# Kernel tuning notes

Hardware: AMD Instinct MI355X
Metric: run time of the kernel (lower is better)

The kernel has to match this reference:

```python
import jax, jax.numpy as jnp
from jax import lax
import numpy as np

S, B, I, H = 1024, 512, 5, 32
G = 4 * H  # torch LSTM gate dim, order: i, f, g, o


def setup_inputs() -> dict:
    key = jax.random.key(0)
    ks = jax.random.split(key, 19)
    n = lambda k, shape, s=0.1: jax.random.normal(k, shape, jnp.float32) * s
    return {
        "x": jax.random.normal(ks[0], (S, B, I), jnp.float32),
        "Wih0": n(ks[1], (G, I)), "Whh0": n(ks[2], (G, H)), "bih0": n(ks[3], (G,)), "bhh0": n(ks[4], (G,)),
        "Wih1": n(ks[5], (G, H)), "Whh1": n(ks[6], (G, H)), "bih1": n(ks[7], (G,)), "bhh1": n(ks[8], (G,)),
        "Wih2": n(ks[9], (G, H)), "Whh2": n(ks[10], (G, H)), "bih2": n(ks[11], (G,)), "bhh2": n(ks[12], (G,)),
        "w1": n(ks[13], (H, H)), "b1": n(ks[14], (H,)),
        "w2": n(ks[15], (H, H)), "b2": n(ks[16], (H,)),
        "w3": n(ks[17], (1, H)), "b3": n(ks[18], (1,)),
    }


def lstm_layer(x, Wih, Whh, bih, bhh):
    # x: [S, B, in]; precompute input projections for all steps (one big GEMM)
    xp = jnp.einsum("sbi,gi->sbg", x, Wih) + bih + bhh  # [S, B, 4H]
    h0 = jnp.zeros((x.shape[1], H), x.dtype)
    c0 = jnp.zeros((x.shape[1], H), x.dtype)

    def step(carry, xg):
        h, c = carry
        gates = xg + h @ Whh.T  # [B, 4H]
        i, f, g, o = jnp.split(gates, 4, axis=-1)
        c = jax.nn.sigmoid(f) * c + jax.nn.sigmoid(i) * jnp.tanh(g)
        h = jax.nn.sigmoid(o) * jnp.tanh(c)
        return (h, c), h

    _, ys = lax.scan(step, (h0, c0), xp)
    return ys  # [S, B, H]


def reference(x, Wih0, Whh0, bih0, bhh0, Wih1, Whh1, bih1, bhh1,
              Wih2, Whh2, bih2, bhh2, w1, b1, w2, b2, w3, b3):
    h = lstm_layer(x, Wih0, Whh0, bih0, bhh0)
    h = lstm_layer(h, Wih1, Whh1, bih1, bhh1)
    h = lstm_layer(h, Wih2, Whh2, bih2, bhh2)  # [S, B, H]
    s, b, hd = h.shape
    y = h.reshape(s * b, hd)
    y = y @ w1.T + b1
    y = y @ w2.T + b2
    y = y @ w3.T + b3
    y = jax.nn.relu(y)
    return y.reshape(s, b, -1)  # [S, B, 1]
```

## Files before the change

### kernel.cpp

```cpp
#include <hip/hip_runtime.h>
#include <math.h>

#define S_LEN 1024
#define BATCH 512
#define HID   32

__device__ __forceinline__ float fast_rcp(float x) { return __builtin_amdgcn_rcpf(x); }

__device__ __forceinline__ float sigmoid_f(float x) {
    return fast_rcp(1.0f + __expf(-x));
}

__device__ __forceinline__ float tanh_f(float x) {
    float t = __expf(-2.0f * fabsf(x));
    float r = (1.0f - t) * fast_rcp(1.0f + t);
    return copysignf(r, x);
}

__global__ __launch_bounds__(192, 2)
void lstm3_fused(const float* __restrict__ x,
                 const float* __restrict__ Wih0, const float* __restrict__ Whh0,
                 const float* __restrict__ bih0, const float* __restrict__ bhh0,
                 const float* __restrict__ Wih1, const float* __restrict__ Whh1,
                 const float* __restrict__ bih1, const float* __restrict__ bhh1,
                 const float* __restrict__ Wih2, const float* __restrict__ Whh2,
                 const float* __restrict__ bih2, const float* __restrict__ bhh2,
                 float* __restrict__ hseq)
{
    const int b = blockIdx.x;
    const int w = threadIdx.x >> 6;
    const int l = threadIdx.x & 63;
    const int j = l & 31;
    const bool lowHalf = (l < 32);
    const int gA = l;
    const int gB = l + 64;

    __shared__ float ring[2][4][HID];
    for (int i = threadIdx.x; i < 2 * 4 * HID; i += 192)
        (&ring[0][0][0])[i] = 0.0f;

    const float* Wih = (w == 0) ? Wih0 : (w == 1) ? Wih1 : Wih2;
    const float* Whh = (w == 0) ? Whh0 : (w == 1) ? Whh1 : Whh2;
    const float* bih = (w == 0) ? bih0 : (w == 1) ? bih1 : bih2;
    const float* bhh = (w == 0) ? bhh0 : (w == 1) ? bhh1 : bhh2;

    float whhA[HID], whhB[HID];
#pragma unroll
    for (int k = 0; k < HID; ++k) {
        whhA[k] = Whh[gA * HID + k];
        whhB[k] = Whh[gB * HID + k];
    }
    float wihA[HID], wihB[HID];
    if (w == 0) {
#pragma unroll
        for (int k = 0; k < 5; ++k) {
            wihA[k] = Wih[gA * 5 + k];
            wihB[k] = Wih[gB * 5 + k];
        }
    } else {
#pragma unroll
        for (int k = 0; k < HID; ++k) {
            wihA[k] = Wih[gA * HID + k];
            wihB[k] = Wih[gB * HID + k];
        }
    }
    const float biasA = bih[gA] + bhh[gA];
    const float biasB = bih[gB] + bhh[gB];

    float c = 0.0f;

    const float* xb0 = x + (size_t)b * 5;
    float xv0 = 0.f, xv1 = 0.f, xv2 = 0.f, xv3 = 0.f, xv4 = 0.f;
    if (w == 0) {
        xv0 = xb0[0]; xv1 = xb0[1]; xv2 = xb0[2]; xv3 = xb0[3]; xv4 = xb0[4];
    }

    __syncthreads();

    for (int t = 0; t < S_LEN + 2; ++t) {
        const int s = t - w;
        const bool active = (s >= 0) && (s < S_LEN);
        const int p = t & 1;

        float aA0 = biasA, aA1 = 0.f, aA2 = 0.f, aA3 = 0.f;
        float aB0 = biasB, aB1 = 0.f, aB2 = 0.f, aB3 = 0.f;

        const float4* hown4 = reinterpret_cast<const float4*>(&ring[p][w + 1][0]);
#pragma unroll
        for (int k4 = 0; k4 < HID / 4; ++k4) {
            float4 hv = hown4[k4];
            aA0 += whhA[4 * k4 + 0] * hv.x;
            aA1 += whhA[4 * k4 + 1] * hv.y;
            aA2 += whhA[4 * k4 + 2] * hv.z;
            aA3 += whhA[4 * k4 + 3] * hv.w;
            aB0 += whhB[4 * k4 + 0] * hv.x;
            aB1 += whhB[4 * k4 + 1] * hv.y;
            aB2 += whhB[4 * k4 + 2] * hv.z;
            aB3 += whhB[4 * k4 + 3] * hv.w;
        }

        if (w == 0) {
            aA0 += wihA[0] * xv0; aB0 += wihB[0] * xv0;
            aA1 += wihA[1] * xv1; aB1 += wihB[1] * xv1;
            aA2 += wihA[2] * xv2; aB2 += wihB[2] * xv2;
            aA3 += wihA[3] * xv3; aB3 += wihB[3] * xv3;
            aA0 += wihA[4] * xv4; aB0 += wihB[4] * xv4;
            if (s + 1 < S_LEN) {
                const float* xn = xb0 + (size_t)(s + 1) * BATCH * 5;
                xv0 = xn[0]; xv1 = xn[1]; xv2 = xn[2]; xv3 = xn[3]; xv4 = xn[4];
            }
        } else {
            const float4* hin4 = reinterpret_cast<const float4*>(&ring[p][w][0]);
#pragma unroll
            for (int k4 = 0; k4 < HID / 4; ++k4) {
                float4 hv = hin4[k4];
                aA0 += wihA[4 * k4 + 0] * hv.x;
                aA1 += wihA[4 * k4 + 1] * hv.y;
                aA2 += wihA[4 * k4 + 2] * hv.z;
                aA3 += wihA[4 * k4 + 3] * hv.w;
                aB0 += wihB[4 * k4 + 0] * hv.x;
                aB1 += wihB[4 * k4 + 1] * hv.y;
                aB2 += wihB[4 * k4 + 2] * hv.z;
                aB3 += wihB[4 * k4 + 3] * hv.w;
            }
        }
        float accA = (aA0 + aA1) + (aA2 + aA3);
        float accB = (aB0 + aB1) + (aB2 + aB3);

        float pA = __shfl_xor(accA, 32);
        float pB = __shfl_xor(accB, 32);
        float gi = lowHalf ? accA : pA;
        float gf = lowHalf ? pA : accA;
        float gg = lowHalf ? accB : pB;
        float go = lowHalf ? pB : accB;

        gi = sigmoid_f(gi);
        gf = sigmoid_f(gf);
        gg = tanh_f(gg);
        go = sigmoid_f(go);
        float c_new = gf * c + gi * gg;
        float h = go * tanh_f(c_new);

        if (active) {
            c = c_new;
            if (lowHalf) {
                ring[p ^ 1][w + 1][j] = h;
                if (w == 2)
                    hseq[((size_t)s * BATCH + b) * HID + j] = h;
            }
        }
        __syncthreads();
    }
}

__global__ __launch_bounds__(256)
void mlp_kernel(const float* __restrict__ h, const float* __restrict__ w1,
                const float* __restrict__ b1, const float* __restrict__ w2,
                const float* __restrict__ b2, const float* __restrict__ w3,
                const float* __restrict__ b3, float* __restrict__ out)
{
    __shared__ float W1[HID * HID];
    __shared__ float W2[HID * HID];
    __shared__ float W3[HID];
    __shared__ float B1[HID];
    __shared__ float B2[HID];
    __shared__ float B3s;

    for (int i = threadIdx.x; i < HID * HID; i += blockDim.x) {
        W1[i] = w1[i];
        W2[i] = w2[i];
    }
    if (threadIdx.x < HID) {
        W3[threadIdx.x] = w3[threadIdx.x];
        B1[threadIdx.x] = b1[threadIdx.x];
        B2[threadIdx.x] = b2[threadIdx.x];
    }
    if (threadIdx.x == 0) B3s = b3[0];
    __syncthreads();

    const size_t e = (size_t)blockIdx.x * blockDim.x + threadIdx.x;
    float hv[HID];
    const float4* hp = reinterpret_cast<const float4*>(h + e * HID);
#pragma unroll
    for (int k4 = 0; k4 < HID / 4; ++k4) {
        float4 v = hp[k4];
        hv[4 * k4 + 0] = v.x;
        hv[4 * k4 + 1] = v.y;
        hv[4 * k4 + 2] = v.z;
        hv[4 * k4 + 3] = v.w;
    }

    float y1[HID];
#pragma unroll
    for (int jj = 0; jj < HID; ++jj) {
        float acc = B1[jj];
#pragma unroll
        for (int k = 0; k < HID; ++k) acc += W1[jj * HID + k] * hv[k];
        y1[jj] = acc;
    }
    float y2[HID];
#pragma unroll
    for (int jj = 0; jj < HID; ++jj) {
        float acc = B2[jj];
#pragma unroll
        for (int k = 0; k < HID; ++k) acc += W2[jj * HID + k] * y1[k];
        y2[jj] = acc;
    }
    float acc3 = B3s;
#pragma unroll
    for (int k = 0; k < HID; ++k) acc3 += W3[k] * y2[k];
    out[e] = fmaxf(acc3, 0.0f);
}

extern "C" void kernel_launch(void* const* d_in, const int* in_sizes, int n_in,
                              void* d_out, int out_size, void* d_ws, size_t ws_size,
                              hipStream_t stream)
{
    const float* x    = (const float*)d_in[0];
    const float* Wih0 = (const float*)d_in[1];
    const float* Whh0 = (const float*)d_in[2];
    const float* bih0 = (const float*)d_in[3];
    const float* bhh0 = (const float*)d_in[4];
    const float* Wih1 = (const float*)d_in[5];
    const float* Whh1 = (const float*)d_in[6];
    const float* bih1 = (const float*)d_in[7];
    const float* bhh1 = (const float*)d_in[8];
    const float* Wih2 = (const float*)d_in[9];
    const float* Whh2 = (const float*)d_in[10];
    const float* bih2 = (const float*)d_in[11];
    const float* bhh2 = (const float*)d_in[12];
    const float* w1   = (const float*)d_in[13];
    const float* b1   = (const float*)d_in[14];
    const float* w2   = (const float*)d_in[15];
    const float* b2   = (const float*)d_in[16];
    const float* w3   = (const float*)d_in[17];
    const float* b3   = (const float*)d_in[18];

    float* hseq = (float*)d_ws;

    lstm3_fused<<<BATCH, 192, 0, stream>>>(x, Wih0, Whh0, bih0, bhh0,
                                           Wih1, Whh1, bih1, bhh1,
                                           Wih2, Whh2, bih2, bhh2, hseq);

    mlp_kernel<<<(S_LEN * BATCH) / 256, 256, 0, stream>>>(hseq, w1, b1, w2, b2, w3, b3,
                                                          (float*)d_out);
}
```

Before: 944.3 us.

## Fold linear MLP head into LSTM kernel and use readlane for recurrent state

The three-layer linear head (no nonlinearity until the final ReLU) is algebraically collapsed into one 32-vector dot product plus a bias. It is computed in the last LSTM wave with a shuffle reduction, so the separate MLP kernel and the hseq round trip through global memory go away. Each wave's own recurrent hidden state is now broadcast with readlane from registers instead of being read from the shared ring, which shrinks the ring to inter-layer handoff only. Risks are small numeric differences from reassociating the head, and the added serial readlane and shuffle latency on the critical path.

New measurement: 956.0 us. Within noise of the previous version (+1.2%).

```diff
diff --git a/kernel.cpp b/kernel.cpp
--- a/kernel.cpp
+++ b/kernel.cpp
@@ -17,15 +17,22 @@
     return copysignf(r, x);
 }
 
+__device__ __forceinline__ float rl(float v, int k) {
+    return __int_as_float(__builtin_amdgcn_readlane(__float_as_int(v), k));
+}
+
 __global__ __launch_bounds__(192, 2)
-void lstm3_fused(const float* __restrict__ x,
-                 const float* __restrict__ Wih0, const float* __restrict__ Whh0,
-                 const float* __restrict__ bih0, const float* __restrict__ bhh0,
-                 const float* __restrict__ Wih1, const float* __restrict__ Whh1,
-                 const float* __restrict__ bih1, const float* __restrict__ bhh1,
-                 const float* __restrict__ Wih2, const float* __restrict__ Whh2,
-                 const float* __restrict__ bih2, const float* __restrict__ bhh2,
-                 float* __restrict__ hseq)
+void lstm3_head(const float* __restrict__ x,
+                const float* __restrict__ Wih0, const float* __restrict__ Whh0,
+                const float* __restrict__ bih0, const float* __restrict__ bhh0,
+                const float* __restrict__ Wih1, const float* __restrict__ Whh1,
+                const float* __restrict__ bih1, const float* __restrict__ bhh1,
+                const float* __restrict__ Wih2, const float* __restrict__ Whh2,
+                const float* __restrict__ bih2, const float* __restrict__ bhh2,
+                const float* __restrict__ w1, const float* __restrict__ b1,
+                const float* __restrict__ w2, const float* __restrict__ b2,
+                const float* __restrict__ w3, const float* __restrict__ b3,
+                float* __restrict__ out)
 {
     const int b = blockIdx.x;
     const int w = threadIdx.x >> 6;
@@ -35,8 +42,8 @@
     const int gA = l;
     const int gB = l + 64;
 
-    __shared__ float ring[2][4][HID];
-    for (int i = threadIdx.x; i < 2 * 4 * HID; i += 192)
+    __shared__ float ring[2][2][HID];
+    for (int i = threadIdx.x; i < 2 * 2 * HID; i += 192)
         (&ring[0][0][0])[i] = 0.0f;
 
     const float* Wih = (w == 0) ? Wih0 : (w == 1) ? Wih1 : Wih2;
@@ -67,61 +74,76 @@
     const float biasA = bih[gA] + bhh[gA];
     const float biasB = bih[gB] + bhh[gB];
 
+    float u_own = 0.0f, beta = 0.0f;
+    if (w == 2) {
+        float t_own = 0.0f;
+#pragma unroll
+        for (int k = 0; k < HID; ++k)
+            t_own += w3[k] * w2[k * HID + j];
+        float uo = 0.0f, bt = 0.0f;
+#pragma unroll
+        for (int k = 0; k < HID; ++k) {
+            float tk = rl(t_own, k);
+            uo += tk * w1[k * HID + j];
+            bt += tk * b1[k] + w3[k] * b2[k];
+        }
+        u_own = uo;
+        beta = bt + b3[0];
+    }
+
     float c = 0.0f;
-
-    const float* xb0 = x + (size_t)b * 5;
+    float h = 0.0f;
+
+    const float* xb = x + (size_t)b * 5;
     float xv0 = 0.f, xv1 = 0.f, xv2 = 0.f, xv3 = 0.f, xv4 = 0.f;
-    if (w == 0) {
-        xv0 = xb0[0]; xv1 = xb0[1]; xv2 = xb0[2]; xv3 = xb0[3]; xv4 = xb0[4];
-    }
+    if (w == 0) { xv0 = xb[0]; xv1 = xb[1]; xv2 = xb[2]; xv3 = xb[3]; xv4 = xb[4]; }
 
     __syncthreads();
 
     for (int t = 0; t < S_LEN + 2; ++t) {
         const int s = t - w;
-        const bool active = (s >= 0) && (s < S_LEN);
+        const bool active = ((unsigned)s < S_LEN);
         const int p = t & 1;
+
+        float4 hin[HID / 4];
+        if (w > 0) {
+            const float4* r4 = reinterpret_cast<const float4*>(&ring[p][w - 1][0]);
+#pragma unroll
+            for (int k4 = 0; k4 < HID / 4; ++k4) hin[k4] = r4[k4];
+        }
 
         float aA0 = biasA, aA1 = 0.f, aA2 = 0.f, aA3 = 0.f;
         float aB0 = biasB, aB1 = 0.f, aB2 = 0.f, aB3 = 0.f;
-
-        const float4* hown4 = reinterpret_cast<const float4*>(&ring[p][w + 1][0]);
-#pragma unroll
-        for (int k4 = 0; k4 < HID / 4; ++k4) {
-            float4 hv = hown4[k4];
-            aA0 += whhA[4 * k4 + 0] * hv.x;
-            aA1 += whhA[4 * k4 + 1] * hv.y;
-            aA2 += whhA[4 * k4 + 2] * hv.z;
-            aA3 += whhA[4 * k4 + 3] * hv.w;
-            aB0 += whhB[4 * k4 + 0] * hv.x;
-            aB1 += whhB[4 * k4 + 1] * hv.y;
-            aB2 += whhB[4 * k4 + 2] * hv.z;
-            aB3 += whhB[4 * k4 + 3] * hv.w;
+#pragma unroll
+        for (int k = 0; k < HID; k += 4) {
+            float h0 = rl(h, k + 0);
+            float h1 = rl(h, k + 1);
+            float h2 = rl(h, k + 2);
+            float h3 = rl(h, k + 3);
+            aA0 += whhA[k + 0] * h0;  aB0 += whhB[k + 0] * h0;
+            aA1 += whhA[k + 1] * h1;  aB1 += whhB[k + 1] * h1;
+            aA2 += whhA[k + 2] * h2;  aB2 += whhB[k + 2] * h2;
+            aA3 += whhA[k + 3] * h3;  aB3 += whhB[k + 3] * h3;
         }
 
         if (w == 0) {
-            aA0 += wihA[0] * xv0; aB0 += wihB[0] * xv0;
-            aA1 += wihA[1] * xv1; aB1 += wihB[1] * xv1;
-            aA2 += wihA[2] * xv2; aB2 += wihB[2] * xv2;
-            aA3 += wihA[3] * xv3; aB3 += wihB[3] * xv3;
-            aA0 += wihA[4] * xv4; aB0 += wihB[4] * xv4;
+            aA0 += wihA[0] * xv0;  aB0 += wihB[0] * xv0;
+            aA1 += wihA[1] * xv1;  aB1 += wihB[1] * xv1;
+            aA2 += wihA[2] * xv2;  aB2 += wihB[2] * xv2;
+            aA3 += wihA[3] * xv3;  aB3 += wihB[3] * xv3;
+            aA0 += wihA[4] * xv4;  aB0 += wihB[4] * xv4;
             if (s + 1 < S_LEN) {
-                const float* xn = xb0 + (size_t)(s + 1) * BATCH * 5;
+                const float* xn = xb + (size_t)(s + 1) * BATCH * 5;
                 xv0 = xn[0]; xv1 = xn[1]; xv2 = xn[2]; xv3 = xn[3]; xv4 = xn[4];
             }
         } else {
-            const float4* hin4 = reinterpret_cast<const float4*>(&ring[p][w][0]);
 #pragma unroll
             for (int k4 = 0; k4 < HID / 4; ++k4) {
-                float4 hv = hin4[k4];
-                aA0 += wihA[4 * k4 + 0] * hv.x;
-                aA1 += wihA[4 * k4 + 1] * hv.y;
-                aA2 += wihA[4 * k4 + 2] * hv.z;
-                aA3 += wihA[4 * k4 + 3] * hv.w;
-                aB0 += wihB[4 * k4 + 0] * hv.x;
-                aB1 += wihB[4 * k4 + 1] * hv.y;
-                aB2 += wihB[4 * k4 + 2] * hv.z;
-                aB3 += wihB[4 * k4 + 3] * hv.w;
+                float4 hv = hin[k4];
+                aA0 += wihA[4 * k4 + 0] * hv.x;  aB0 += wihB[4 * k4 + 0] * hv.x;
+                aA1 += wihA[4 * k4 + 1] * hv.y;  aB1 += wihB[4 * k4 + 1] * hv.y;
+                aA2 += wihA[4 * k4 + 2] * hv.z;  aB2 += wihB[4 * k4 + 2] * hv.z;
+                aA3 += wihA[4 * k4 + 3] * hv.w;  aB3 += wihB[4 * k4 + 3] * hv.w;
             }
         }
         float accA = (aA0 + aA1) + (aA2 + aA3);
@@ -139,77 +161,25 @@
         gg = tanh_f(gg);
         go = sigmoid_f(go);
         float c_new = gf * c + gi * gg;
-        float h = go * tanh_f(c_new);
+        float h_new = go * tanh_f(c_new);
 
         if (active) {
             c = c_new;
-            if (lowHalf) {
-                ring[p ^ 1][w + 1][j] = h;
-                if (w == 2)
-                    hseq[((size_t)s * BATCH + b) * HID + j] = h;
+            h = h_new;
+            if (w < 2) {
+                if (lowHalf) ring[p ^ 1][w][j] = h_new;
+            } else {
+                float prt = u_own * h_new;
+                prt += __shfl_xor(prt, 1);
+                prt += __shfl_xor(prt, 2);
+                prt += __shfl_xor(prt, 4);
+                prt += __shfl_xor(prt, 8);
+                prt += __shfl_xor(prt, 16);
+                if (l == 0) out[(size_t)s * BATCH + b] = fmaxf(prt + beta, 0.0f);
             }
         }
         __syncthreads();
     }
-}
-
-__global__ __launch_bounds__(256)
-void mlp_kernel(const float* __restrict__ h, const float* __restrict__ w1,
-                const float* __restrict__ b1, const float* __restrict__ w2,
-                const float* __restrict__ b2, const float* __restrict__ w3,
-                const float* __restrict__ b3, float* __restrict__ out)
-{
-    __shared__ float W1[HID * HID];
-    __shared__ float W2[HID * HID];
-    __shared__ float W3[HID];
-    __shared__ float B1[HID];
-    __shared__ float B2[HID];
-    __shared__ float B3s;
-
-    for (int i = threadIdx.x; i < HID * HID; i += blockDim.x) {
-        W1[i] = w1[i];
-        W2[i] = w2[i];
-    }
-    if (threadIdx.x < HID) {
-        W3[threadIdx.x] = w3[threadIdx.x];
-        B1[threadIdx.x] = b1[threadIdx.x];
-        B2[threadIdx.x] = b2[threadIdx.x];
-    }
-    if (threadIdx.x == 0) B3s = b3[0];
-    __syncthreads();
-
-    const size_t e = (size_t)blockIdx.x * blockDim.x + threadIdx.x;
-    float hv[HID];
-    const float4* hp = reinterpret_cast<const float4*>(h + e * HID);
-#pragma unroll
-    for (int k4 = 0; k4 < HID / 4; ++k4) {
-        float4 v = hp[k4];
-        hv[4 * k4 + 0] = v.x;
-        hv[4 * k4 + 1] = v.y;
-        hv[4 * k4 + 2] = v.z;
-        hv[4 * k4 + 3] = v.w;
-    }
-
-    float y1[HID];
-#pragma unroll
-    for (int jj = 0; jj < HID; ++jj) {
-        float acc = B1[jj];
-#pragma unroll
-        for (int k = 0; k < HID; ++k) acc += W1[jj * HID + k] * hv[k];
-        y1[jj] = acc;
-    }
-    float y2[HID];
-#pragma unroll
-    for (int jj = 0; jj < HID; ++jj) {
-        float acc = B2[jj];
-#pragma unroll
-        for (int k = 0; k < HID; ++k) acc += W2[jj * HID + k] * y1[k];
-        y2[jj] = acc;
-    }
-    float acc3 = B3s;
-#pragma unroll
-    for (int k = 0; k < HID; ++k) acc3 += W3[k] * y2[k];
-    out[e] = fmaxf(acc3, 0.0f);
 }
 
 extern "C" void kernel_launch(void* const* d_in, const int* in_sizes, int n_in,
@@ -236,12 +206,9 @@
     const float* w3   = (const float*)d_in[17];
     const float* b3   = (const float*)d_in[18];
 
-    float* hseq = (float*)d_ws;
-
-    lstm3_fused<<<BATCH, 192, 0, stream>>>(x, Wih0, Whh0, bih0, bhh0,
-                                           Wih1, Whh1, bih1, bhh1,
-                                           Wih2, Whh2, bih2, bhh2, hseq);
-
-    mlp_kernel<<<(S_LEN * BATCH) / 256, 256, 0, stream>>>(hseq, w1, b1, w2, b2, w3, b3,
-                                                          (float*)d_out);
-}
+    lstm3_head<<<BATCH, 192, 0, stream>>>(x, Wih0, Whh0, bih0, bhh0,
+                                          Wih1, Whh1, bih1, bhh1,
+                                          Wih2, Whh2, bih2, bhh2,
+                                          w1, b1, w2, b2, w3, b3,
+                                          (float*)d_out);
+}
```
